# Optimization experiments

Hardware: AMD Instinct MI355X
Metric: run time of the kernel (lower is better)

Reference implementation:

```python
import jax, jax.numpy as jnp
import numpy as np

BN_EPS = 1e-5
SLOPE = 0.2  # LeakyReLU negative slope
LOCAL_POINTS = 512


def knn_idx(x, k):
    # x: [B, C, N] -> [B, N, k] indices of k nearest neighbors (incl. self)
    xx = jnp.sum(x * x, axis=1)                       # [B, N]
    inner = jnp.einsum('bcn,bcm->bnm', x, x)          # [B, N, N]
    neg_d2 = 2.0 * inner - xx[:, :, None] - xx[:, None, :]
    return jax.lax.top_k(neg_d2, k)[1]


def edge_conv(x, k, w1, b1, g, be, w2, b2):
    # EdgeConv: knn gather -> (center - neigh, center) -> 1x1 conv -> BN -> LeakyReLU -> 1x1 conv -> max over k
    B, C, N = x.shape
    idx = knn_idx(x, k)                               # [B, N, k]
    xt = jnp.transpose(x, (0, 2, 1))                  # [B, N, C]
    neigh = xt[jnp.arange(B)[:, None, None], idx]     # [B, N, k, C]
    neigh = jnp.transpose(neigh, (0, 3, 1, 2))        # [B, C, N, k]
    center = jnp.broadcast_to(x[:, :, :, None], neigh.shape)
    feat = jnp.concatenate([center - neigh, center], axis=1)  # [B, 2C, N, k]
    h = jnp.einsum('oc,bcnk->bonk', w1, feat) + b1[None, :, None, None]
    mu = jnp.mean(h, axis=(0, 2, 3), keepdims=True)   # train-mode BatchNorm2d
    var = jnp.mean((h - mu) ** 2, axis=(0, 2, 3), keepdims=True)
    h = (h - mu) / jnp.sqrt(var + BN_EPS) * g[None, :, None, None] + be[None, :, None, None]
    h = jnp.where(h >= 0, h, SLOPE * h)
    h = jnp.einsum('oc,bcnk->bonk', w2, h) + b2[None, :, None, None]
    return jnp.max(h, axis=-1)                        # [B, out, N]


def fps(xyz, m):
    # furthest point sampling; xyz: [B, N, 3] -> [B, m] int indices; starts at index 0 (CUDA convention)
    B, N, _ = xyz.shape
    idx0 = jnp.zeros((B, m), jnp.int32)
    dists0 = jnp.full((B, N), 1e10, jnp.float32)
    last0 = jnp.zeros((B,), jnp.int32)

    def body(i, carry):
        idx, dists, last = carry
        p = jnp.take_along_axis(xyz, last[:, None, None], axis=1)  # [B, 1, 3]
        d = jnp.sum((xyz - p) ** 2, axis=-1)                       # [B, N]
        dists = jnp.minimum(dists, d)
        nxt = jnp.argmax(dists, axis=1).astype(jnp.int32)
        return idx.at[:, i].set(nxt), dists, nxt

    idx, _, _ = jax.lax.fori_loop(1, m, body, (idx0, dists0, last0))
    return idx


def setup_inputs():
    key = jax.random.key(0)
    ks = jax.random.split(key, 13)
    B, N = 32, 2048
    x = jax.random.normal(ks[0], (B, 3, N), jnp.float32)

    def w(k, o, c):
        return jax.random.normal(k, (o, c), jnp.float32) * (1.0 / np.sqrt(c))

    inp = {'x': x}
    dims = [(3, 64), (64, 256), (256, 512)]
    for li, (ci, co) in enumerate(dims, start=1):
        inp[f'w{li}a'] = w(ks[4 * li - 3], co // 2, 2 * ci)
        inp[f'b{li}a'] = jnp.zeros((co // 2,), jnp.float32)
        inp[f'g{li}'] = jnp.ones((co // 2,), jnp.float32)
        inp[f'be{li}'] = jnp.zeros((co // 2,), jnp.float32)
        inp[f'w{li}b'] = w(ks[4 * li - 2], co, co // 2)
        inp[f'b{li}b'] = jnp.zeros((co,), jnp.float32)
    return inp


def reference(x, w1a, b1a, g1, be1, w1b, b1b, w2a, b2a, g2, be2, w2b, b2b, w3a, b3a, g3, be3, w3b, b3b):
    x1 = edge_conv(x, 16, w1a, b1a, g1, be1, w1b, b1b)        # [B, 64, N]
    idx = fps(jnp.transpose(x, (0, 2, 1)), LOCAL_POINTS)       # [B, M]
    x1 = jnp.take_along_axis(x1, idx[:, None, :], axis=2)      # gather_points -> [B, 64, M]
    x2 = edge_conv(x1, 8, w2a, b2a, g2, be2, w2b, b2b)         # [B, 256, M]
    x3 = edge_conv(x2, 4, w3a, b3a, g3, be3, w3b, b3b)         # [B, 512, M]
    return jnp.concatenate([x1, x2, x3], axis=1)               # [B, 832, M]
```

## Files before the change

kernel.cpp:

```cpp
#include <hip/hip_runtime.h>
#include <hip/hip_bf16.h>
#include <cstddef>


constexpr size_t OFF_IDX1 = 0;
constexpr size_t OFF_IDX2 = OFF_IDX1 + 1048576;
constexpr size_t OFF_IDX3 = OFF_IDX2 + 131072;
constexpr size_t OFF_FPS  = OFF_IDX3 + 65536;
constexpr size_t OFF_ST   = OFF_FPS + 16384;
constexpr size_t OFF_SS1  = OFF_ST + 1664;
constexpr size_t OFF_SS2  = OFF_SS1 + 64;
constexpr size_t OFF_SS3  = OFF_SS2 + 256;
constexpr size_t OFF_NORM = OFF_SS3 + 512;
constexpr size_t OFF_X1F  = OFF_NORM + 32768;

__global__ __launch_bounds__(256) void knn3d3_kernel(const float* __restrict__ x,
                                                     int* __restrict__ idx)
{
    constexpr int N = 2048, QB = 64, NS = 4, MS = N / NS , KK = 16;
    __shared__ __align__(16) double smem[5120];
    float*  sx  = (float*)smem;
    float*  sy  = sx + 2048;
    float*  sz  = sy + 2048;
    double* snd = smem + 3072;
    double* mv  = smem;
    unsigned short* mi = (unsigned short*)(smem + 4096);

    int t = threadIdx.x;
    int q = t >> 2, s = t & 3;
    int b  = blockIdx.x >> 5;
    int n0 = (blockIdx.x & 31) << 6;
    int n  = n0 + q;
    const float* xb = x + (size_t)b * 3 * N;

    for (int e = t; e < N; e += 256) {
        float mx = xb[e], my = xb[N + e], mz = xb[2 * N + e];
        sx[e] = mx; sy[e] = my; sz[e] = mz;
        double dx = (double)mx, dy = (double)my, dz = (double)mz;
        snd[e] = dx * dx + dy * dy + dz * dz;
    }
    __syncthreads();

    double qx = (double)sx[n], qy = (double)sy[n], qz = (double)sz[n];
    double qq = snd[n];
    double bv[KK]; int bi[KK];
#pragma unroll
    for (int j = 0; j < KK; ++j) { bv[j] = -1e300; bi[j] = 0; }

#pragma unroll 4
    for (int i = 0; i < MS; ++i) {
        int mm = (i + s * 8) & (MS - 1);
        int m  = s * MS + mm;
        double dot = qx * (double)sx[m] + qy * (double)sy[m] + qz * (double)sz[m];
        double val = 2.0 * dot - qq - snd[m];
        if (val > bv[KK - 1]) {
            bv[KK - 1] = val; bi[KK - 1] = m;
#pragma unroll
            for (int j = KK - 1; j > 0; --j) {
                if (bv[j] > bv[j - 1]) {
                    double tv = bv[j]; bv[j] = bv[j - 1]; bv[j - 1] = tv;
                    int    ti = bi[j]; bi[j] = bi[j - 1]; bi[j - 1] = ti;
                }
            }
        }
    }
    __syncthreads();
#pragma unroll
    for (int j = 0; j < KK; ++j) {
        mv[(q * NS + s) * KK + j] = bv[j];
        mi[(q * NS + s) * KK + j] = (unsigned short)bi[j];
    }
    __syncthreads();
    if (t < QB) {
        int qq2 = t;
        double hv[NS]; int hj[NS];
#pragma unroll
        for (int s2 = 0; s2 < NS; ++s2) { hv[s2] = mv[(qq2 * NS + s2) * KK]; hj[s2] = 0; }
        int* op = idx + ((size_t)(b * N) + n0 + qq2) * KK;
#pragma unroll
        for (int r = 0; r < KK; ++r) {
            double best = -1e301; int bs = 0;
#pragma unroll
            for (int s2 = 0; s2 < NS; ++s2) {
                if (hv[s2] > best) { best = hv[s2]; bs = s2; }
            }
#pragma unroll
            for (int s2 = 0; s2 < NS; ++s2) {
                if (s2 == bs) {
                    op[r] = (int)mi[(qq2 * NS + s2) * KK + hj[s2]];
                    hj[s2]++;
                    hv[s2] = (hj[s2] < KK) ? mv[(qq2 * NS + s2) * KK + hj[s2]] : -1e301;
                }
            }
        }
    }
}

__global__ __launch_bounds__(256) void stats1_kernel(const float* __restrict__ x,
                                                     const int* __restrict__ idx1,
                                                     const float* __restrict__ w1,
                                                     const float* __restrict__ b1,
                                                     double* __restrict__ stats)
{
    __shared__ float wl[32][9];
    __shared__ float bsh[32];
    __shared__ float red[2][4][32];
    int t = threadIdx.x;
    for (int e = t; e < 192; e += 256) wl[e / 6][e % 6] = w1[e];
    if (t < 32) bsh[t] = b1[t];
    __syncthreads();

    float sum[32], sq[32];
#pragma unroll
    for (int o = 0; o < 32; o++) { sum[o] = 0.f; sq[o] = 0.f; }

    int base = blockIdx.x * 256 + t;
    for (int it = 0; it < 16; ++it) {
        int p = base + it * 65536;
        int b = p >> 15, rem = p & 32767, n = rem >> 4;
        int m = idx1[p];
        const float* xb = x + (size_t)b * 3 * 2048;
        float cx = xb[n], cy = xb[2048 + n], cz = xb[4096 + n];
        float f0 = cx - xb[m], f1 = cy - xb[2048 + m], f2 = cz - xb[4096 + m];
#pragma unroll
        for (int o = 0; o < 32; o++) {
            float h = bsh[o] + wl[o][0] * f0 + wl[o][1] * f1 + wl[o][2] * f2
                             + wl[o][3] * cx + wl[o][4] * cy + wl[o][5] * cz;
            sum[o] += h; sq[o] += h * h;
        }
    }
    int lane = t & 63, wv = t >> 6;
#pragma unroll
    for (int o = 0; o < 32; o++) {
        float s = sum[o], q = sq[o];
#pragma unroll
        for (int d = 1; d < 64; d <<= 1) { s += __shfl_xor(s, d); q += __shfl_xor(q, d); }
        if (lane == 0) { red[0][wv][o] = s; red[1][wv][o] = q; }
    }
    __syncthreads();
    if (t < 32) {
        atomicAdd(&stats[t], (double)(red[0][0][t] + red[0][1][t] + red[0][2][t] + red[0][3][t]));
    } else if (t < 64) {
        int o = t - 32;
        atomicAdd(&stats[32 + o], (double)(red[1][0][o] + red[1][1][o] + red[1][2][o] + red[1][3][o]));
    }
}

__global__ void finalize_kernel(const double* __restrict__ stats,
                                const float* __restrict__ g,
                                const float* __restrict__ be,
                                float* __restrict__ scsh, int co2, double invcnt)
{
    int t = threadIdx.x;
    if (t < co2) {
        double mu  = stats[t] * invcnt;
        double var = stats[co2 + t] * invcnt - mu * mu;
        float  sc  = (float)((double)g[t] / sqrt(var + 1e-5));
        scsh[t]       = sc;
        scsh[co2 + t] = be[t] - (float)mu * sc;
    }
}

__global__ __launch_bounds__(256) void passB1_kernel(const float* __restrict__ x,
                                                     const int* __restrict__ idx1,
                                                     const float* __restrict__ w1,
                                                     const float* __restrict__ b1,
                                                     const float* __restrict__ scsh,
                                                     const float* __restrict__ w2,
                                                     const float* __restrict__ b2,
                                                     float* __restrict__ x1full)
{
    __shared__ float hn[256][36];
    __shared__ float wl[32][9];
    __shared__ float sc[32], sh[32], bs1[32];
    int t = threadIdx.x;
    int b = blockIdx.x >> 7, nt = blockIdx.x & 127;
    int n0 = nt << 4;
    for (int e = t; e < 192; e += 256) wl[e / 6][e % 6] = w1[e];
    if (t < 32) { sc[t] = scsh[t]; sh[t] = scsh[32 + t]; bs1[t] = b1[t]; }
    __syncthreads();
    {
        int n = n0 + (t >> 4), kk = t & 15;
        int pix = (((b << 11) + n) << 4) + kk;
        int m = idx1[pix];
        const float* xb = x + (size_t)b * 3 * 2048;
        float cx = xb[n], cy = xb[2048 + n], cz = xb[4096 + n];
        float f0 = cx - xb[m], f1 = cy - xb[2048 + m], f2 = cz - xb[4096 + m];
#pragma unroll
        for (int o = 0; o < 32; o++) {
            float h = bs1[o] + wl[o][0] * f0 + wl[o][1] * f1 + wl[o][2] * f2
                             + wl[o][3] * cx + wl[o][4] * cy + wl[o][5] * cz;
            h = h * sc[o] + sh[o];
            hn[t][o] = (h >= 0.f) ? h : 0.2f * h;
        }
    }
    __syncthreads();
    int o2 = t & 63, ng = t >> 6;
    float w2r[32];
#pragma unroll
    for (int c = 0; c < 32; c++) w2r[c] = w2[o2 * 32 + c];
    float bb = b2[o2];
#pragma unroll
    for (int ns = 0; ns < 4; ns++) {
        int nl = ng * 4 + ns;
        float mx = -1e30f;
#pragma unroll
        for (int kk = 0; kk < 16; kk++) {
            const float* hp = &hn[(nl << 4) + kk][0];
            float s = 0.f;
#pragma unroll
            for (int c4 = 0; c4 < 8; c4++) {
                float4 f = *(const float4*)(hp + c4 * 4);
                s += w2r[c4 * 4] * f.x + w2r[c4 * 4 + 1] * f.y
                   + w2r[c4 * 4 + 2] * f.z + w2r[c4 * 4 + 3] * f.w;
            }
            mx = fmaxf(mx, s);
        }
        x1full[((size_t)(b << 11) + n0 + nl) * 64 + o2] = mx + bb;
    }
}

__global__ __launch_bounds__(256) void fps2_kernel(const float* __restrict__ x,
                                                   int* __restrict__ fpsidx)
{
    constexpr int N = 2048;
    int b = blockIdx.x, t = threadIdx.x;
    int lane = t & 63, wv = t >> 6;
    const float* xb = x + (size_t)b * 3 * N;
    __shared__ __align__(16) float4 sxyz[N];
    __shared__ double redv[2][4];
    __shared__ int    redi[2][4];

    float px[8], py[8], pz[8];
    double dd[8];
#pragma unroll
    for (int j = 0; j < 8; j++) {
        int n = j * 256 + t;
        float a = xb[n], bb = xb[N + n], c = xb[2 * N + n];
        px[j] = a; py[j] = bb; pz[j] = c; dd[j] = 1e10;
        sxyz[n] = make_float4(a, bb, c, 0.f);
    }
    __syncthreads();
    if (t == 0) fpsidx[(size_t)b * 512] = 0;
    int last = 0;

    for (int i = 1; i < 512; i++) {
        float4 lp = sxyz[last];
        double lpx = (double)lp.x, lpy = (double)lp.y, lpz = (double)lp.z;
        double v[8];
#pragma unroll
        for (int j = 0; j < 8; j++) {
            double dx = (double)px[j] - lpx, dy = (double)py[j] - lpy, dz = (double)pz[j] - lpz;
            double d = dx * dx + dy * dy + dz * dz;
            double nd = fmin(dd[j], d);
            dd[j] = nd; v[j] = nd;
        }
        double a0 = v[0], a1 = v[1], a2 = v[2], a3 = v[3];
        int    i0 = t,    i1 = 256 + t, i2 = 512 + t, i3 = 768 + t;
        if (v[4] > a0) { a0 = v[4]; i0 = 1024 + t; }
        if (v[5] > a1) { a1 = v[5]; i1 = 1280 + t; }
        if (v[6] > a2) { a2 = v[6]; i2 = 1536 + t; }
        if (v[7] > a3) { a3 = v[7]; i3 = 1792 + t; }
        if (a2 > a0) { a0 = a2; i0 = i2; }
        if (a3 > a1) { a1 = a3; i1 = i3; }
        if (a1 > a0) { a0 = a1; i0 = i1; }
        double bestd = a0; int bestn = i0;
#pragma unroll
        for (int s = 1; s < 64; s <<= 1) {
            double od = __shfl_xor(bestd, s);
            int    on = __shfl_xor(bestn, s);
            if (od > bestd || (od == bestd && on < bestn)) { bestd = od; bestn = on; }
        }
        int buf = i & 1;
        if (lane == 0) { redv[buf][wv] = bestd; redi[buf][wv] = bestn; }
        __syncthreads();
        double fb = redv[buf][0]; int fn = redi[buf][0];
#pragma unroll
        for (int w2 = 1; w2 < 4; w2++) {
            double ov = redv[buf][w2]; int on = redi[buf][w2];
            if (ov > fb || (ov == fb && on < fn)) { fb = ov; fn = on; }
        }
        last = fn;
        if (t == 0) fpsidx[(size_t)b * 512 + i] = fn;
    }
}

__global__ __launch_bounds__(256) void gather_kernel(const float* __restrict__ x1full,
                                                     const int* __restrict__ fpsidx,
                                                     float* __restrict__ out)
{
    int e = blockIdx.x * 256 + threadIdx.x;
    int j = e & 511; int rest = e >> 9; int c = rest & 63; int b = rest >> 6;
    int fj = fpsidx[b * 512 + j];
    out[((size_t)b * 832 + c) * 512 + j] = x1full[((size_t)(b << 11) + fj) * 64 + c];
}

template <int C>
__global__ __launch_bounds__(256) void norms_kernel(const float* __restrict__ xin,
                                                    size_t xbstride,
                                                    double* __restrict__ norms)
{
    int b = blockIdx.x >> 1;
    int n = ((blockIdx.x & 1) << 8) + threadIdx.x;
    const float* xb = xin + (size_t)b * xbstride;
    double s = 0.0;
    for (int c = 0; c < C; c++) { double v = (double)xb[(size_t)c * 512 + n]; s += v * v; }
    norms[(b << 9) + n] = s;
}

template <int C, int KK>
__global__ __launch_bounds__(256) void knn_feat2_kernel(const float* __restrict__ xin,
                                                        size_t xbstride,
                                                        const double* __restrict__ norms,
                                                        int* __restrict__ idxout)
{
    constexpr int NN = 512, QB = 16, NS = 16, MS = NN / NS , CC = 16;
    constexpr int CHUNKS = C / CC;
    __shared__ __align__(16) double smem[4736];
    float*  sm = (float*)smem;
    float*  sq = (float*)(smem + 4096);
    double* sn = smem + 4224;
    double* mv = smem;
    int*    mi = (int*)(smem + (size_t)QB * NS * KK);

    int t = threadIdx.x;
    int q = t & 15, s = t >> 4;
    int b  = blockIdx.x >> 5;
    int n0 = (blockIdx.x & 31) << 4;
    int n  = n0 + q;
    const float* xb = xin + (size_t)b * xbstride;

    for (int e = t; e < NN; e += 256) sn[e] = norms[(b << 9) + e];

    double acc[MS];
#pragma unroll
    for (int i = 0; i < MS; ++i) acc[i] = 0.0;

    for (int ch = 0; ch < CHUNKS; ++ch) {
        int c0 = ch * CC;
        __syncthreads();
        for (int e = t; e < CC * NN; e += 256) {
            int c = e >> 9, m = e & 511;
            sm[c * NN + m] = xb[(size_t)(c0 + c) * NN + m];
        }
        {
            int c = t >> 4, qq = t & 15;
            sq[c * QB + qq] = xb[(size_t)(c0 + c) * NN + n0 + qq];
        }
        __syncthreads();
        double qv[CC];
#pragma unroll
        for (int cc = 0; cc < CC; ++cc) qv[cc] = (double)sq[cc * QB + q];
#pragma unroll
        for (int m4 = 0; m4 < MS / 4; ++m4) {
#pragma unroll
            for (int cc = 0; cc < CC; ++cc) {
                float4 f = *(const float4*)&sm[cc * NN + s * MS + m4 * 4];
                acc[m4 * 4 + 0] += qv[cc] * (double)f.x;
                acc[m4 * 4 + 1] += qv[cc] * (double)f.y;
                acc[m4 * 4 + 2] += qv[cc] * (double)f.z;
                acc[m4 * 4 + 3] += qv[cc] * (double)f.w;
            }
        }
    }

    double nq = sn[n];
    double bv[KK]; int bi[KK];
#pragma unroll
    for (int j = 0; j < KK; ++j) { bv[j] = -1e300; bi[j] = 0; }
#pragma unroll
    for (int mm = 0; mm < MS; ++mm) {
        int m = s * MS + mm;
        double val = 2.0 * acc[mm] - nq - sn[m];
        if (val > bv[KK - 1]) {
            bv[KK - 1] = val; bi[KK - 1] = m;
#pragma unroll
            for (int j = KK - 1; j > 0; --j) {
                if (bv[j] > bv[j - 1]) {
                    double tv = bv[j]; bv[j] = bv[j - 1]; bv[j - 1] = tv;
                    int    ti = bi[j]; bi[j] = bi[j - 1]; bi[j - 1] = ti;
                }
            }
        }
    }
    __syncthreads();
#pragma unroll
    for (int j = 0; j < KK; ++j) {
        mv[(q * NS + s) * KK + j] = bv[j];
        mi[(q * NS + s) * KK + j] = bi[j];
    }
    __syncthreads();
    if (t < QB) {
        int qq2 = t;
        double hv[NS]; int hj[NS];
#pragma unroll
        for (int s2 = 0; s2 < NS; ++s2) { hv[s2] = mv[(qq2 * NS + s2) * KK]; hj[s2] = 0; }
        int* op = idxout + ((size_t)(b * NN) + n0 + qq2) * KK;
#pragma unroll
        for (int r = 0; r < KK; ++r) {
            double best = -1e301; int bs = 0;
#pragma unroll
            for (int s2 = 0; s2 < NS; ++s2) {
                if (hv[s2] > best) { best = hv[s2]; bs = s2; }
            }
#pragma unroll
            for (int s2 = 0; s2 < NS; ++s2) {
                if (s2 == bs) {
                    op[r] = mi[(qq2 * NS + s2) * KK + hj[s2]];
                    hj[s2]++;
                    hv[s2] = (hj[s2] < KK) ? mv[(qq2 * NS + s2) * KK + hj[s2]] : -1e301;
                }
            }
        }
    }
}

template <int C, int CO2, bool BF16OUT>
__global__ __launch_bounds__(256) void gh_kernel(const float* __restrict__ xin,
                                                 size_t xbstride,
                                                 const float* __restrict__ w1,
                                                 const float* __restrict__ b1,
                                                 void* __restrict__ Gout,
                                                 void* __restrict__ Hout)
{
    constexpr int TN = 128, TO = 64, KC = 16, NN = 512;
    __shared__ float xs[KC][TN];
    __shared__ float wls[KC][TO];
    __shared__ float wus[KC][TO];
    int t = threadIdx.x;
    constexpr int ntiles = NN / TN, otiles = CO2 / TO;
    int bid = blockIdx.x;
    int b = bid / (ntiles * otiles);
    int rem = bid % (ntiles * otiles);
    int n0 = (rem / otiles) * TN;
    int o0 = (rem % otiles) * TO;
    const float* xb = xin + (size_t)b * xbstride;

    int tn = t & 15, to = t >> 4;
    float accG[4][8], accH[4][8];
#pragma unroll
    for (int i = 0; i < 4; i++)
#pragma unroll
        for (int j = 0; j < 8; j++) { accG[i][j] = 0.f; accH[i][j] = 0.f; }

    for (int c0 = 0; c0 < C; c0 += KC) {
        __syncthreads();
        for (int e = t; e < KC * TN; e += 256) {
            int c = e >> 7, n = e & 127;
            xs[c][n] = xb[(size_t)(c0 + c) * NN + n0 + n];
        }
        for (int e = t; e < KC * TO; e += 256) {
            int o = e >> 4, c = e & 15;
            float wl = w1[(size_t)(o0 + o) * (2 * C) + c0 + c];
            float wr = w1[(size_t)(o0 + o) * (2 * C) + C + c0 + c];
            wls[c][o] = wl;
            wus[c][o] = wl + wr;
        }
        __syncthreads();
#pragma unroll 4
        for (int c = 0; c < KC; ++c) {
            float xv[8], wlv[4], wuv[4];
#pragma unroll
            for (int j = 0; j < 8; j++) xv[j] = xs[c][tn + j * 16];
#pragma unroll
            for (int i = 0; i < 4; i++) { wlv[i] = wls[c][to + i * 16]; wuv[i] = wus[c][to + i * 16]; }
#pragma unroll
            for (int i = 0; i < 4; i++)
#pragma unroll
                for (int j = 0; j < 8; j++) {
                    accG[i][j] += wuv[i] * xv[j];
                    accH[i][j] += wlv[i] * xv[j];
                }
        }
    }
#pragma unroll
    for (int i = 0; i < 4; i++) {
        int o = o0 + to + i * 16;
        float bb = b1[o];
#pragma unroll
        for (int j = 0; j < 8; j++) {
            int n = n0 + tn + j * 16;
            size_t off = ((size_t)b * NN + n) * CO2 + o;
            if constexpr (BF16OUT) {
                ((__hip_bfloat16*)Gout)[off] = __float2bfloat16(accG[i][j] + bb);
                ((__hip_bfloat16*)Hout)[off] = __float2bfloat16(accH[i][j]);
            } else {
                ((float*)Gout)[off] = accG[i][j] + bb;
                ((float*)Hout)[off] = accH[i][j];
            }
        }
    }
}

template <int CO2, int KK, bool STATS, bool GHBF>
__global__ __launch_bounds__(CO2) void edge2_kernel(
    const void* __restrict__ Gin, const void* __restrict__ Hin,
    const int* __restrict__ idx,
    double* __restrict__ stats,
    const float* __restrict__ scsh, const float* __restrict__ w2,
    const float* __restrict__ b2,
    float* __restrict__ outp, size_t obstride, int tiles_per_block)
{
    constexpr int NN = 512, CCH = 16, TP = 32, TN = TP / KK;
    __shared__ float wtl[STATS ? 1 : CCH][STATS ? 1 : (CO2 + 1)];
    __shared__ float hn[STATS ? 1 : TP * CO2];
    __shared__ int   smidx[TP];
    int t = threadIdx.x;
    float ssum = 0.f, ssq = 0.f;

    for (int ti = 0; ti < tiles_per_block; ++ti) {
        int tileIdx = blockIdx.x * tiles_per_block + ti;
        int b = tileIdx / (NN / TN), nt = tileIdx % (NN / TN);
        int n0 = nt * TN;
        __syncthreads();
        if (t < TP) {
            int n = n0 + t / KK, kk = t % KK;
            smidx[t] = idx[((size_t)(b * NN) + n) * KK + kk];
        }
        __syncthreads();

        float h[TP];
#pragma unroll
        for (int p = 0; p < TP; p++) {
            int n = n0 + p / KK;
            int m = smidx[p];
            size_t go = ((size_t)b * NN + n) * CO2 + t;
            size_t ho = ((size_t)b * NN + m) * CO2 + t;
            float gv, hv;
            if constexpr (GHBF) {
                gv = __bfloat162float(((const __hip_bfloat16*)Gin)[go]);
                hv = __bfloat162float(((const __hip_bfloat16*)Hin)[ho]);
            } else {
                gv = ((const float*)Gin)[go];
                hv = ((const float*)Hin)[ho];
            }
            h[p] = gv - hv;
        }

        if constexpr (STATS) {
#pragma unroll
            for (int p = 0; p < TP; p++) { ssum += h[p]; ssq += h[p] * h[p]; }
        } else {
            float scv = scsh[t], shv = scsh[CO2 + t];
#pragma unroll
            for (int p = 0; p < TP; p++) {
                float v = h[p] * scv + shv;
                hn[p * CO2 + t] = (v >= 0.f) ? v : 0.2f * v;
            }
            for (int g = 0; g < 2; ++g) {
                float s[TP];
#pragma unroll
                for (int p = 0; p < TP; p++) s[p] = 0.f;
                for (int ch = 0; ch < CO2 / CCH; ++ch) {
                    int c0 = ch * CCH;
                    __syncthreads();
                    for (int e = t; e < CCH * CO2; e += CO2) {
                        int o = e / CCH, ci = e % CCH;
                        wtl[ci][o] = w2[((size_t)(g * CO2 + o)) * CO2 + c0 + ci];
                    }
                    __syncthreads();
#pragma unroll
                    for (int c4 = 0; c4 < CCH / 4; c4++) {
                        float a0 = wtl[c4 * 4][t], a1 = wtl[c4 * 4 + 1][t];
                        float a2 = wtl[c4 * 4 + 2][t], a3 = wtl[c4 * 4 + 3][t];
#pragma unroll
                        for (int p = 0; p < TP; p++) {
                            const float4 f = *(const float4*)&hn[p * CO2 + c0 + c4 * 4];
                            s[p] += a0 * f.x + a1 * f.y + a2 * f.z + a3 * f.w;
                        }
                    }
                }
                float bb2 = b2[g * CO2 + t];
#pragma unroll
                for (int nl = 0; nl < TN; ++nl) {
                    float mx = s[nl * KK];
#pragma unroll
                    for (int kk = 1; kk < KK; ++kk) mx = fmaxf(mx, s[nl * KK + kk]);
                    outp[(size_t)b * obstride + (size_t)(g * CO2 + t) * NN + n0 + nl] = mx + bb2;
                }
            }
        }
    }
    if constexpr (STATS) {
        atomicAdd(&stats[t], (double)ssum);
        atomicAdd(&stats[CO2 + t], (double)ssq);
    }
}

extern "C" void kernel_launch(void* const* d_in, const int* in_sizes, int n_in,
                              void* d_out, int out_size, void* d_ws, size_t ws_size,
                              hipStream_t stream)
{
    const float* x   = (const float*)d_in[0];
    const float* w1a = (const float*)d_in[1];
    const float* b1a = (const float*)d_in[2];
    const float* g1  = (const float*)d_in[3];
    const float* be1 = (const float*)d_in[4];
    const float* w1b = (const float*)d_in[5];
    const float* b1b = (const float*)d_in[6];
    const float* w2a = (const float*)d_in[7];
    const float* b2a = (const float*)d_in[8];
    const float* g2  = (const float*)d_in[9];
    const float* be2 = (const float*)d_in[10];
    const float* w2b = (const float*)d_in[11];
    const float* b2b = (const float*)d_in[12];
    const float* w3a = (const float*)d_in[13];
    const float* b3a = (const float*)d_in[14];
    const float* g3  = (const float*)d_in[15];
    const float* be3 = (const float*)d_in[16];
    const float* w3b = (const float*)d_in[17];
    const float* b3b = (const float*)d_in[18];

    float* out = (float*)d_out;
    float* fws = (float*)d_ws;
    int*    idx1   = (int*)(fws + OFF_IDX1);
    int*    idx2   = (int*)(fws + OFF_IDX2);
    int*    idx3   = (int*)(fws + OFF_IDX3);
    int*    fpsidx = (int*)(fws + OFF_FPS);
    double* st1 = (double*)(fws + OFF_ST);
    double* st2 = st1 + 64;
    double* st3 = st2 + 256;
    float*  ss1 = fws + OFF_SS1;
    float*  ss2 = fws + OFF_SS2;
    float*  ss3 = fws + OFF_SS3;
    double* nrm = (double*)(fws + OFF_NORM);
    float*  x1full = fws + OFF_X1F;
    float*  G2 = fws + OFF_X1F;
    float*  H2 = G2 + 2097152;
    __hip_bfloat16* G3 = (__hip_bfloat16*)(fws + OFF_X1F);
    __hip_bfloat16* H3 = (__hip_bfloat16*)(fws + OFF_X1F + 2097152);

    const size_t OB = 832 * 512;

    hipMemsetAsync(st1, 0, 832 * sizeof(double), stream);

    knn3d3_kernel<<<1024, 256, 0, stream>>>(x, idx1);
    stats1_kernel<<<256, 256, 0, stream>>>(x, idx1, w1a, b1a, st1);
    finalize_kernel<<<1, 256, 0, stream>>>(st1, g1, be1, ss1, 32, 1.0 / 1048576.0);
    passB1_kernel<<<4096, 256, 0, stream>>>(x, idx1, w1a, b1a, ss1, w1b, b1b, x1full);

    fps2_kernel<<<32, 256, 0, stream>>>(x, fpsidx);
    gather_kernel<<<4096, 256, 0, stream>>>(x1full, fpsidx, out);

    norms_kernel<64><<<64, 256, 0, stream>>>(out, OB, nrm);
    knn_feat2_kernel<64, 8><<<1024, 256, 0, stream>>>(out, OB, nrm, idx2);
    gh_kernel<64, 128, false><<<256, 256, 0, stream>>>(out, OB, w2a, b2a, G2, H2);
    edge2_kernel<128, 8, true, false><<<512, 128, 0, stream>>>(
        G2, H2, idx2, st2, nullptr, nullptr, nullptr, nullptr, 0, 8);
    finalize_kernel<<<1, 256, 0, stream>>>(st2, g2, be2, ss2, 128, 1.0 / 131072.0);
    edge2_kernel<128, 8, false, false><<<4096, 128, 0, stream>>>(
        G2, H2, idx2, nullptr, ss2, w2b, b2b, out + 64 * 512, OB, 1);

    norms_kernel<256><<<64, 256, 0, stream>>>(out + 64 * 512, OB, nrm);
    knn_feat2_kernel<256, 4><<<1024, 256, 0, stream>>>(out + 64 * 512, OB, nrm, idx3);
    gh_kernel<256, 256, true><<<512, 256, 0, stream>>>(out + 64 * 512, OB, w3a, b3a, G3, H3);
    edge2_kernel<256, 4, true, true><<<512, 256, 0, stream>>>(
        G3, H3, idx3, st3, nullptr, nullptr, nullptr, nullptr, 0, 4);
    finalize_kernel<<<1, 256, 0, stream>>>(st3, g3, be3, ss3, 256, 1.0 / 65536.0);
    edge2_kernel<256, 4, false, true><<<2048, 256, 0, stream>>>(
        G3, H3, idx3, nullptr, ss3, w3b, b3b, out + 320 * 512, OB, 1);
}
```

Measured before the change: 2.476 ms.

## Use bf16 MFMA for the layer-3 second conv and max-over-k

```diff
diff --git a/kernel.cpp b/kernel.cpp
--- a/kernel.cpp
+++ b/kernel.cpp
@@ -2,6 +2,9 @@
 #include <hip/hip_bf16.h>
 #include <cstddef>
 
+
+typedef __bf16 bf16x8 __attribute__((ext_vector_type(8)));
+typedef float  f32x4  __attribute__((ext_vector_type(4)));
 
 constexpr size_t OFF_IDX1 = 0;
 constexpr size_t OFF_IDX2 = OFF_IDX1 + 1048576;
@@ -13,6 +16,7 @@
 constexpr size_t OFF_SS3  = OFF_SS2 + 256;
 constexpr size_t OFF_NORM = OFF_SS3 + 512;
 constexpr size_t OFF_X1F  = OFF_NORM + 32768;
+constexpr size_t OFF_W3BF = OFF_X1F + 4194304;
 
 __global__ __launch_bounds__(256) void knn3d3_kernel(const float* __restrict__ x,
                                                      int* __restrict__ idx)
@@ -159,6 +163,14 @@
         scsh[t]       = sc;
         scsh[co2 + t] = be[t] - (float)mu * sc;
     }
+}
+
+__global__ __launch_bounds__(256) void cvt_bf16_kernel(const float* __restrict__ src,
+                                                       __hip_bfloat16* __restrict__ dst,
+                                                       int n)
+{
+    int i = blockIdx.x * 256 + threadIdx.x;
+    if (i < n) dst[i] = __float2bfloat16(src[i]);
 }
 
 __global__ __launch_bounds__(256) void passB1_kernel(const float* __restrict__ x,
@@ -584,6 +596,89 @@
     if constexpr (STATS) {
         atomicAdd(&stats[t], (double)ssum);
         atomicAdd(&stats[CO2 + t], (double)ssq);
+    }
+}
+
+__global__ __launch_bounds__(256) void edge3_mfma_kernel(
+    const __hip_bfloat16* __restrict__ G, const __hip_bfloat16* __restrict__ H,
+    const int* __restrict__ idx, const float* __restrict__ scsh,
+    const __hip_bfloat16* __restrict__ w3bf, const float* __restrict__ b2,
+    float* __restrict__ outp, size_t obstride)
+{
+    constexpr int NN = 512, CO2 = 256, TP = 32, PTS = 8, PITCH = 264;
+    __shared__ __align__(16) unsigned short hnb[TP * PITCH];
+    __shared__ int smidx[TP];
+    int t = threadIdx.x;
+    int b  = blockIdx.x >> 6;
+    int pg = blockIdx.x & 63;
+    int n0 = pg * PTS;
+
+    if (t < TP) smidx[t] = idx[((size_t)(b * NN) + n0 + (t >> 2)) * 4 + (t & 3)];
+    __syncthreads();
+
+    {
+        float scv = scsh[t], shv = scsh[CO2 + t];
+        const __hip_bfloat16* Gb = G + (size_t)b * NN * CO2;
+        const __hip_bfloat16* Hb = H + (size_t)b * NN * CO2;
+#pragma unroll
+        for (int pt = 0; pt < PTS; ++pt) {
+            float gv = __bfloat162float(Gb[(size_t)(n0 + pt) * CO2 + t]);
+#pragma unroll
+            for (int ks = 0; ks < 4; ++ks) {
+                int p = pt * 4 + ks;
+                int m = smidx[p];
+                float hv = __bfloat162float(Hb[(size_t)m * CO2 + t]);
+                float v = (gv - hv) * scv + shv;
+                v = (v >= 0.f) ? v : 0.2f * v;
+                __hip_bfloat16 bv = __float2bfloat16(v);
+                hnb[p * PITCH + t] = *reinterpret_cast<unsigned short*>(&bv);
+            }
+        }
+    }
+    __syncthreads();
+
+    int l = t & 63, wv = t >> 6;
+    int lr = l & 15, lk = l >> 4;
+    f32x4 acc[8][2];
+#pragma unroll
+    for (int i = 0; i < 8; i++)
+#pragma unroll
+        for (int j = 0; j < 2; j++) acc[i][j] = (f32x4){0.f, 0.f, 0.f, 0.f};
+
+    int o_wv = wv * 128;
+    for (int kk = 0; kk < 8; ++kk) {
+        int koff = kk * 32 + lk * 8;
+        bf16x8 bfrag[2];
+#pragma unroll
+        for (int nt = 0; nt < 2; ++nt)
+            bfrag[nt] = *reinterpret_cast<const bf16x8*>(&hnb[(nt * 16 + lr) * PITCH + koff]);
+#pragma unroll
+        for (int mt = 0; mt < 8; ++mt) {
+            bf16x8 afrag = *reinterpret_cast<const bf16x8*>(
+                &w3bf[(size_t)(o_wv + mt * 16 + lr) * CO2 + koff]);
+#pragma unroll
+            for (int nt = 0; nt < 2; ++nt)
+                acc[mt][nt] = __builtin_amdgcn_mfma_f32_16x16x32_bf16(
+                    afrag, bfrag[nt], acc[mt][nt], 0, 0, 0);
+        }
+    }
+
+#pragma unroll
+    for (int mt = 0; mt < 8; ++mt) {
+#pragma unroll
+        for (int nt = 0; nt < 2; ++nt) {
+#pragma unroll
+            for (int r = 0; r < 4; ++r) {
+                float v = acc[mt][nt][r];
+                v = fmaxf(v, __shfl_xor(v, 1));
+                v = fmaxf(v, __shfl_xor(v, 2));
+                if ((lr & 3) == 0) {
+                    int o   = o_wv + mt * 16 + lk * 4 + r;
+                    int pnt = n0 + nt * 4 + (lr >> 2);
+                    outp[(size_t)b * obstride + (size_t)o * NN + pnt] = v + b2[o];
+                }
+            }
+        }
     }
 }
 
@@ -629,10 +724,12 @@
     float*  H2 = G2 + 2097152;
     __hip_bfloat16* G3 = (__hip_bfloat16*)(fws + OFF_X1F);
     __hip_bfloat16* H3 = (__hip_bfloat16*)(fws + OFF_X1F + 2097152);
+    __hip_bfloat16* w3bf = (__hip_bfloat16*)(fws + OFF_W3BF);
 
     const size_t OB = 832 * 512;
 
     hipMemsetAsync(st1, 0, 832 * sizeof(double), stream);
+    cvt_bf16_kernel<<<512, 256, 0, stream>>>(w3b, w3bf, 512 * 256);
 
     knn3d3_kernel<<<1024, 256, 0, stream>>>(x, idx1);
     stats1_kernel<<<256, 256, 0, stream>>>(x, idx1, w1a, b1a, st1);
@@ -657,6 +754,6 @@
     edge2_kernel<256, 4, true, true><<<512, 256, 0, stream>>>(
         G3, H3, idx3, st3, nullptr, nullptr, nullptr, nullptr, 0, 4);
     finalize_kernel<<<1, 256, 0, stream>>>(st3, g3, be3, ss3, 256, 1.0 / 65536.0);
-    edge2_kernel<256, 4, false, true><<<2048, 256, 0, stream>>>(
-        G3, H3, idx3, nullptr, ss3, w3b, b3b, out + 320 * 512, OB, 1);
-}
+    edge3_mfma_kernel<<<2048, 256, 0, stream>>>(
+        G3, H3, idx3, ss3, w3bf, b3b, out + 320 * 512, OB);
+}
```

Measured after the change: 2.110 ms. 14.8% less time.
